# Kernel optimization log

Measured on AMD Instinct MI355X. Metric: run time of the kernel, lower is better.

The kernel has to match this reference:

```python
import jax, jax.numpy as jnp
import numpy as np
from jax import lax

B, L, D = 8, 2048, 512
K = 16            # cysteines per sequence (fixed by construction)
CYS = 4           # AA2ID['C']
CW = 5            # disulfide_context_window
KW = 2 * CW + 1   # conv kernel size = 11
H = D // 2        # LSTM hidden per direction = 256
STR = 0.4         # cys_optimization_strength


def setup_inputs() -> dict:
    key = jax.random.key(0)
    ks = jax.random.split(key, 16)
    hidden_states = jax.random.normal(ks[0], (B, L, D), jnp.float32)
    # amino-acid ids with exactly K cysteines per sequence, spaced > KW apart
    aa = jax.random.randint(ks[1], (B, L), 0, 20)
    aa = jnp.where(aa == CYS, 5, aa)
    base = 64 + 128 * jnp.arange(K)
    jitter = jax.random.randint(ks[2], (B, K), -40, 41)
    pos = base[None, :] + jitter  # [B,K], strictly increasing, gaps > 11
    aa_ids = aa.at[jnp.arange(B)[:, None], pos].set(CYS)
    s = 0.05
    W_bil = jax.random.normal(ks[3], (128, D, D)) * s
    b_bil = jax.random.normal(ks[4], (128,)) * s
    cls_w1 = jax.random.normal(ks[5], (64, 128)) * s
    cls_b1 = jax.random.normal(ks[6], (64,)) * s
    cls_w2 = jax.random.normal(ks[7], (1, 64)) * s
    cls_b2 = jax.random.normal(ks[8], (1,)) * s
    # 2 layers x 2 directions; both layers have input size D (2*H == D)
    lstm_Wih = jax.random.normal(ks[9], (2, 2, 4 * H, D)) * s
    lstm_Whh = jax.random.normal(ks[10], (2, 2, 4 * H, H)) * s
    lstm_bih = jax.random.normal(ks[11], (2, 2, 4 * H)) * s
    lstm_bhh = jax.random.normal(ks[12], (2, 2, 4 * H)) * s
    conv_w = jax.random.normal(ks[13], (D, D, KW)) * 0.02
    conv_b = jax.random.normal(ks[14], (D,)) * 0.02
    dsb_factor = jax.random.normal(ks[15], (D,)) * 0.1
    return dict(hidden_states=hidden_states, aa_ids=aa_ids, W_bil=W_bil,
                b_bil=b_bil, cls_w1=cls_w1, cls_b1=cls_b1, cls_w2=cls_w2,
                cls_b2=cls_b2, lstm_Wih=lstm_Wih, lstm_Whh=lstm_Whh,
                lstm_bih=lstm_bih, lstm_bhh=lstm_bhh, conv_w=conv_w,
                conv_b=conv_b, dsb_factor=dsb_factor)


def _lstm_dir(x, Wih, Whh, bih, bhh, reverse):
    # x: [B,L,In] -> [B,L,H]; PyTorch gate order i,f,g,o
    bsz = x.shape[0]
    xs = jnp.swapaxes(x, 0, 1)  # [L,B,In]
    if reverse:
        xs = xs[::-1]

    def step(carry, xt):
        h, c = carry
        g = xt @ Wih.T + h @ Whh.T + bih + bhh  # [B,4H]
        i, f, gg, o = jnp.split(g, 4, axis=-1)
        c = jax.nn.sigmoid(f) * c + jax.nn.sigmoid(i) * jnp.tanh(gg)
        h = jax.nn.sigmoid(o) * jnp.tanh(c)
        return (h, c), h

    init = (jnp.zeros((bsz, H), x.dtype), jnp.zeros((bsz, H), x.dtype))
    _, hs = lax.scan(step, init, xs)
    if reverse:
        hs = hs[::-1]
    return jnp.swapaxes(hs, 0, 1)


def _bilstm(x, Wih, Whh, bih, bhh):
    out = x
    for layer in range(2):  # dropout inactive in eval mode
        fw = _lstm_dir(out, Wih[layer, 0], Whh[layer, 0], bih[layer, 0], bhh[layer, 0], False)
        bw = _lstm_dir(out, Wih[layer, 1], Whh[layer, 1], bih[layer, 1], bhh[layer, 1], True)
        out = jnp.concatenate([fw, bw], axis=-1)
    return out


def reference(hidden_states, aa_ids, W_bil, b_bil, cls_w1, cls_b1, cls_w2,
              cls_b2, lstm_Wih, lstm_Whh, lstm_bih, lstm_bhh, conv_w, conv_b,
              dsb_factor):
    dt = hidden_states.dtype
    cys_mask = (aa_ids == CYS)  # [B,L] bool, exactly K per row
    pos = jax.vmap(lambda m: jnp.nonzero(m, size=K, fill_value=0)[0])(cys_mask)  # [B,K]

    # ---- batched bilinear + classifier over all cys pairs ----
    feats = jnp.take_along_axis(hidden_states, pos[:, :, None], axis=1)  # [B,K,D]
    t = jnp.einsum('bkd,cde->bkce', feats, W_bil)            # [B,K,128,D]
    pf = jnp.einsum('bkce,bme->bkmc', t, feats) + b_bil      # [B,K,K,128]
    h1 = jax.nn.relu(pf @ cls_w1.T + cls_b1)
    prob = jax.nn.sigmoid(h1 @ cls_w2.T + cls_b2)[..., 0]    # [B,K,K]
    dist = jnp.abs(pos[:, :, None] - pos[:, None, :])
    prob = jnp.where(dist < 2, prob * 0.1, prob)

    # ---- greedy NMS-style pair selection (prob desc, prob > 0.5, no reuse) ----
    iu, ju = jnp.triu_indices(K, k=1)  # P = K*(K-1)/2 pairs
    probs_flat = prob[:, iu, ju]       # [B,P]

    def greedy(pflat):
        order = jnp.argsort(-pflat)
        ii, jj, pp = iu[order], ju[order], pflat[order]

        def step(used, trip):
            i, j, p = trip
            sel = jnp.logical_and(jnp.logical_and(~used[i], ~used[j]), p > 0.5)
            used = used.at[i].set(used[i] | sel)
            used = used.at[j].set(used[j] | sel)
            return used, sel

        _, sels = lax.scan(step, jnp.zeros(K, bool), (ii, jj, pp))
        return jnp.zeros(iu.shape[0], bool).at[order].set(sels)

    sel_flat = jax.vmap(greedy)(probs_flat)
    sel_mat = jnp.zeros((B, K, K), bool).at[:, iu, ju].set(sel_flat)

    # ---- redox LSTM + windowed cys enhancement ----
    opt = _bilstm(hidden_states, lstm_Wih, lstm_Whh, lstm_bih, lstm_bhh)  # [B,L,D]
    cm = cys_mask.astype(dt)
    cov = lax.conv_general_dilated(cm[:, None, :], jnp.ones((1, 1, KW), dt),
                                   (1,), ((CW, CW),),
                                   dimension_numbers=('NCH', 'OIH', 'NCH'))[:, 0, :]
    win = (cov > 0).astype(dt)  # [B,L] 1 where within CW of a cysteine
    cys_enh = hidden_states + STR * opt * win[..., None] + dsb_factor * cm[..., None]

    # ---- local structure conv ----
    struct = lax.conv_general_dilated(jnp.swapaxes(cys_enh, 1, 2), conv_w,
                                      (1,), ((CW, CW),),
                                      dimension_numbers=('NCH', 'OIH', 'NCH'))
    struct = jnp.swapaxes(struct + conv_b[None, :, None], 1, 2)

    output = hidden_states + 0.3 * (cys_enh - hidden_states) + 0.2 * (struct - hidden_states)
    return (output, prob, sel_mat)
```

## Files before the change

kernel.cpp:

```cpp
#include <hip/hip_runtime.h>
#include <hip/hip_bf16.h>

typedef float  f32x4 __attribute__((ext_vector_type(4)));
typedef float  f32x2 __attribute__((ext_vector_type(2)));
typedef int    i32x4 __attribute__((ext_vector_type(4)));
typedef int    i32x8 __attribute__((ext_vector_type(8)));

#define NB   8
#define LSEQ 2048
#define DDIM 512
#define KC   16

__device__ __forceinline__ float rcp_(float x){ return __builtin_amdgcn_rcpf(x); }
__device__ __forceinline__ float ex2_(float x){ return __builtin_amdgcn_exp2f(x); }
__device__ __forceinline__ float clamp60(float x){ return fminf(fmaxf(x, -60.f), 60.f); }
__device__ __forceinline__ unsigned pk2(float a, float b){
    __hip_bfloat16 x=__float2bfloat16(a), y=__float2bfloat16(b);
    return (unsigned)*(unsigned short*)&x | ((unsigned)*(unsigned short*)&y<<16);
}

#define GLDS(gp, lp) __builtin_amdgcn_global_load_lds(                      \
    (__attribute__((address_space(1))) const void*)(gp),                   \
    (__attribute__((address_space(3))) void*)(lp), 16, 0, 0)

__global__ __launch_bounds__(256) void k_prep(const float* __restrict__ hidden, __hip_bfloat16* __restrict__ hbf,
                                              const float* __restrict__ Wih, __hip_bfloat16* __restrict__ wihbf,
                                              const float* __restrict__ bih, const float* __restrict__ bhh,
                                              float* __restrict__ bias2,
                                              const float* __restrict__ convw, __hip_bfloat16* __restrict__ wtc,
                                              const int* __restrict__ aa, int* __restrict__ pos,
                                              float* __restrict__ cm, float* __restrict__ win,
                                              int* __restrict__ cnt){
    int bid = blockIdx.x, tid = threadIdx.x;
    if(bid < 4096){
        size_t i = (size_t)bid*256 + tid;
        const f32x4* s = (const f32x4*)(hidden + i*8);
        f32x4 v0 = s[0], v1 = s[1];
        i32x4 o; o.x = pk2(v0.x,v0.y); o.y = pk2(v0.z,v0.w);
                 o.z = pk2(v1.x,v1.y); o.w = pk2(v1.z,v1.w);
        ((i32x4*)hbf)[i] = o;
    } else if(bid < 5120){
        size_t i = (size_t)(bid-4096)*256 + tid;
        const f32x4* s = (const f32x4*)(Wih + i*8);
        f32x4 v0 = s[0], v1 = s[1];
        i32x4 o; o.x = pk2(v0.x,v0.y); o.y = pk2(v0.z,v0.w);
                 o.z = pk2(v1.x,v1.y); o.w = pk2(v1.z,v1.w);
        ((i32x4*)wihbf)[i] = o;
    } else if(bid < 5136){
        int i = (bid-5120)*256 + tid;
        bias2[i] = bih[i] + bhh[i];
    } else if(bid < 6160){
        int idx = (bid-5136)*256 + tid;
        #pragma unroll
        for(int tap=0; tap<11; ++tap)
            wtc[(size_t)tap*262144 + idx] = __float2bfloat16(convw[(size_t)idx*11 + tap]);
    } else if(bid < 6168){
        int b = bid - 6160;
        __shared__ unsigned char fl[LSEQ];
        for(int t=tid; t<LSEQ; t+=256) fl[t] = (aa[b*LSEQ+t]==4) ? 1 : 0;
        __syncthreads();
        if(tid==0){
            int c=0;
            for(int t=0; t<LSEQ && c<KC; ++t) if(fl[t]) pos[b*KC + c++] = t;
            for(; c<KC; ++c) pos[b*KC+c]=0;
        }
        for(int t=tid; t<LSEQ; t+=256){
            cm[b*LSEQ+t] = fl[t] ? 1.f : 0.f;
            int lo = t-5 < 0 ? 0 : t-5;
            int hi = t+5 > LSEQ-1 ? LSEQ-1 : t+5;
            float wv = 0.f;
            for(int u=lo; u<=hi; ++u) if(fl[u]) wv = 1.f;
            win[b*LSEQ+t] = wv;
        }
    } else {
        if(tid < 256) cnt[tid] = 0;
    }
}

__device__ __forceinline__ void gemm_body(char* smem, const __hip_bfloat16* __restrict__ A,
        const __hip_bfloat16* __restrict__ Bw, const float* __restrict__ bias,
        __hip_bfloat16* __restrict__ C, int* __restrict__ cnt, int g){
    const int KD = 512, N = 2048;
    int nt = g & 15;
    int j  = g >> 4;
    int kpos = j >> 3, bat = j & 7;
    int mt = bat*16 + ((kpos&1) ? (15 - (kpos>>1)) : (kpos>>1));
    __hip_bfloat16 (*As)[32] = (__hip_bfloat16(*)[32])smem;
    __hip_bfloat16 (*Bs)[32] = (__hip_bfloat16(*)[32])(smem + 8192);
    int tid = threadIdx.x, w = tid>>6, lane = tid&63, lo = lane&15, hi = lane>>4;
    int wm = w>>1, wn = w&1;
    f32x4 acc[2][4];
    #pragma unroll
    for(int s=0;s<2;s++){
        #pragma unroll
        for(int t2=0;t2<4;t2++) acc[s][t2] = (f32x4){0.f,0.f,0.f,0.f};
    }
    int lr = tid>>2, lc = (tid&3)*8;
    const __hip_bfloat16* Ab = A  + (size_t)(mt*128)*KD;
    const __hip_bfloat16* Bb = Bw + (size_t)(nt*128)*KD;
    for(int kk=0; kk<KD; kk+=32){
        __builtin_amdgcn_s_barrier();
        GLDS(Ab + (size_t)lr*KD + kk + lc, &As[lr][lc]);
        GLDS(Bb + (size_t)lr*KD + kk + lc, &Bs[lr][lc]);
        asm volatile("s_waitcnt vmcnt(0)" ::: "memory");
        __builtin_amdgcn_s_barrier();
        i32x4 av[2], bv[4];
        #pragma unroll
        for(int s=0;s<2;s++) av[s] = *(const i32x4*)(&As[wm*32+s*16+lo][hi*8]);
        #pragma unroll
        for(int t2=0;t2<4;t2++) bv[t2] = *(const i32x4*)(&Bs[wn*64+t2*16+lo][hi*8]);
        asm volatile("s_nop 1" ::);
        #pragma unroll
        for(int s=0;s<2;s++){
            #pragma unroll
            for(int t2=0;t2<4;t2++)
                asm volatile("v_mfma_f32_16x16x32_bf16 %0, %1, %2, %0" : "+v"(acc[s][t2]) : "v"(av[s]), "v"(bv[t2]));
        }
    }
    asm volatile("s_nop 7\n\ts_nop 7" ::);
    #pragma unroll
    for(int t2=0;t2<4;t2++){
        int n = nt*128 + wn*64 + t2*16 + lo;
        float bn = bias[n];
        #pragma unroll
        for(int s=0;s<2;s++){
            #pragma unroll
            for(int rr=0;rr<4;rr++){
                int m = mt*128 + wm*32 + s*16 + hi*4 + rr;
                C[(size_t)m*N + n] = __float2bfloat16(acc[s][t2][rr] + bn);
            }
        }
    }
    asm volatile("s_waitcnt vmcnt(0)" ::: "memory");
    __syncthreads();
    if(tid==0)
        __hip_atomic_fetch_add(cnt + mt, 1, __ATOMIC_RELEASE, __HIP_MEMORY_SCOPE_AGENT);
}

__device__ __forceinline__ void recur_body(char* smem, const float* __restrict__ Whh,
        const __hip_bfloat16* __restrict__ Gx, __hip_bfloat16* __restrict__ Hout,
        const int* __restrict__ cnt, int layer, int bat, int dir){
    unsigned char (*hb)[256]    = (unsigned char(*)[256])smem;
    __hip_bfloat16 (*gxs)[1024] = (__hip_bfloat16(*)[1024])(smem + 512);
    const int tid = threadIdx.x, w = tid>>6, lane = tid&63, lo = lane&15, hi = lane>>4;
    for(int i=tid; i<128; i+=512) ((int*)smem)[i] = 0;

    i32x8 bf[8][2];
    const float* wbase = Whh + ((size_t)(layer*2 + dir)*1024)*256;
    #pragma unroll
    for(int q=0;q<4;q++){
        #pragma unroll
        for(int s=0;s<2;s++){
            int j = q*256 + w*32 + s*16 + lo;
            const float* wr = wbase + (size_t)j*256;
            #pragma unroll
            for(int c=0;c<2;c++){
                i32x8 v;
                #pragma unroll
                for(int u=0; u<8; ++u){
                    f32x4 wv = *(const f32x4*)(wr + c*128 + hi*32 + u*4);
                    int pk = __builtin_amdgcn_cvt_pk_fp8_f32(wv.x, wv.y, 0, false);
                    pk = __builtin_amdgcn_cvt_pk_fp8_f32(wv.z, wv.w, pk, true);
                    v[u] = pk;
                }
                bf[q*2+s][c] = v;
            }
        }
    }
    const int pm = w*32 + ((hi&1)<<4) + lo;
    float cst = 0.f;
    const __hip_bfloat16* gxbase = Gx + (size_t)bat*LSEQ*2048 + dir*1024;
    const int cbase = bat*16;
    int mtr = -1;

    {
        int tok0 = dir ? (LSEQ-1) : 0;
        int tok1 = dir ? (LSEQ-2) : 1;
        if(w < 2){
            int mtn = cbase + (tok0>>7);
            if(lane==0){
                while(__hip_atomic_load(cnt+mtn, __ATOMIC_ACQUIRE, __HIP_MEMORY_SCOPE_AGENT) < 16)
                    __builtin_amdgcn_s_sleep(2);
            }
            mtr = mtn;
            GLDS(gxbase + (size_t)tok0*2048 + w*512 + lane*8, &gxs[0][w*512]);
            GLDS(gxbase + (size_t)tok1*2048 + w*512 + lane*8, &gxs[1][w*512]);
        }
    }
    asm volatile("s_waitcnt vmcnt(0) lgkmcnt(0)" ::: "memory");
    __builtin_amdgcn_s_barrier();
    __builtin_amdgcn_sched_barrier(0);

    int cur = 0;
    for(int t=0; t<LSEQ; ++t){
        const int tt = dir ? (LSEQ-1-t) : t;
        const int hcur = t&1, hnxt = hcur^1;
        int nx2 = cur+2; if(nx2>=3) nx2-=3;
        float xi = __bfloat162float(gxs[cur][      pm]);
        float xf = __bfloat162float(gxs[cur][256 + pm]);
        float xg = __bfloat162float(gxs[cur][512 + pm]);
        float xo = __bfloat162float(gxs[cur][768 + pm]);
        {
            int tp = (t+2 < LSEQ) ? (t+2) : (LSEQ-1);
            int tok = dir ? (LSEQ-1-tp) : tp;
            if(w < 2){
                int mtn = cbase + (tok>>7);
                if(mtn != mtr){
                    if(lane==0){
                        while(__hip_atomic_load(cnt+mtn, __ATOMIC_ACQUIRE, __HIP_MEMORY_SCOPE_AGENT) < 16)
                            __builtin_amdgcn_s_sleep(2);
                    }
                    mtr = mtn;
                }
                GLDS(gxbase + (size_t)tok*2048 + w*512 + lane*8, &gxs[nx2][w*512]);
            }
        }
        i32x8 af[2];
        #pragma unroll
        for(int c=0;c<2;c++){
            i32x4 v0 = *(const i32x4*)(&hb[hcur][c*128 + hi*32]);
            i32x4 v1 = *(const i32x4*)(&hb[hcur][c*128 + hi*32 + 16]);
            af[c] = __builtin_shufflevector(v0, v1, 0,1,2,3,4,5,6,7);
        }
        f32x4 aa[8], ab[8];
        #pragma unroll
        for(int i=0;i<8;i++){ aa[i] = (f32x4){0.f,0.f,0.f,0.f}; ab[i] = (f32x4){0.f,0.f,0.f,0.f}; }
        asm volatile("s_nop 1" ::);
        #pragma unroll
        for(int i=0;i<8;i++)
            asm volatile("v_mfma_f32_16x16x128_f8f6f4 %0, %1, %2, %0"
                         : "+v"(aa[i]) : "v"(af[0]), "a"(bf[i][0]));
        #pragma unroll
        for(int i=0;i<8;i++)
            asm volatile("v_mfma_f32_16x16x128_f8f6f4 %0, %1, %2, %0"
                         : "+v"(ab[i]) : "v"(af[1]), "a"(bf[i][1]));
        asm volatile("s_nop 7\n\ts_nop 7" ::);
        {
            float aI = (hi&1) ? (aa[1][0]+ab[1][0]) : (aa[0][0]+ab[0][0]);
            float aF = (hi&1) ? (aa[3][0]+ab[3][0]) : (aa[2][0]+ab[2][0]);
            float aG = (hi&1) ? (aa[5][0]+ab[5][0]) : (aa[4][0]+ab[4][0]);
            float aO = (hi&1) ? (aa[7][0]+ab[7][0]) : (aa[6][0]+ab[6][0]);
            float gi = aI + xi;
            float gf = aF + xf;
            float gg = aG + xg;
            float go = aO + xo;
            float sf = rcp_(1.f + ex2_(gf * -1.44269504f));
            float ag = ex2_(clamp60(gg * 2.88539008f));
            float bi = ex2_(clamp60(gi * -1.44269504f));
            float it = (ag - 1.f) * rcp_((1.f + bi) * (ag + 1.f));
            float c  = sf*cst + it;
            cst = c;
            float ac = ex2_(clamp60(c * 2.88539008f));
            float bo = ex2_(clamp60(go * -1.44269504f));
            float h  = (ac - 1.f) * rcp_((1.f + bo) * (ac + 1.f));
            if(hi < 2){
                int pk = __builtin_amdgcn_cvt_pk_fp8_f32(h, h, 0, false);
                hb[hnxt][pm] = (unsigned char)(pk & 0xff);
                Hout[((size_t)bat*LSEQ + tt)*512 + dir*256 + pm] = __float2bfloat16(h);
            }
        }
        asm volatile("s_waitcnt vmcnt(2) lgkmcnt(0)" ::: "memory");
        __builtin_amdgcn_s_barrier();
        __builtin_amdgcn_sched_barrier(0);
        cur = (cur+1 == 3) ? 0 : cur+1;
    }
}

__device__ __forceinline__ void bilinear_body(char* smem, const float* __restrict__ hidden,
        const int* __restrict__ pos, const float* __restrict__ Wb, const float* __restrict__ bb,
        float* __restrict__ pf, int idx){
    int c = idx & 127, b = idx >> 7;
    float (*fl)[516] = (float(*)[516])smem;
    float (*tl)[516] = (float(*)[516])(smem + 33024);
    int tid = threadIdx.x;
    for(int i=tid; i<2048; i+=512){
        int k = i>>7, d = (i&127)*4;
        int p = pos[b*KC + k];
        f32x4 v = *(const f32x4*)(hidden + ((size_t)b*LSEQ + p)*DDIM + d);
        fl[k][d]=v.x; fl[k][d+1]=v.y; fl[k][d+2]=v.z; fl[k][d+3]=v.w;
    }
    __syncthreads();
    int e = tid;
    float acc[16];
    #pragma unroll
    for(int k=0;k<16;k++) acc[k]=0.f;
    const float* wc = Wb + (size_t)c*512*512;
    for(int d=0; d<512; ++d){
        float wv = wc[(size_t)d*512 + e];
        #pragma unroll
        for(int k=0;k<16;k++) acc[k] += fl[k][d]*wv;
    }
    #pragma unroll
    for(int k=0;k<16;k++) tl[k][e] = acc[k];
    __syncthreads();
    if(tid < 256){
        int kq = tid>>4, mq = tid&15;
        const f32x4* tp = (const f32x4*)&tl[kq][0];
        const f32x4* fp = (const f32x4*)&fl[mq][0];
        float s = 0.f;
        #pragma unroll 8
        for(int e2=0;e2<128;e2++){ f32x4 a=tp[e2], v=fp[e2]; s += a.x*v.x + a.y*v.y + a.z*v.z + a.w*v.w; }
        pf[(((size_t)b*16+kq)*16+mq)*128 + c] = s + bb[c];
    }
}

__device__ __forceinline__ void clsgreedy_body(char* smem, const float* __restrict__ pf,
        const float* __restrict__ w1, const float* __restrict__ b1,
        const float* __restrict__ w2, const float* __restrict__ b2,
        const int* __restrict__ pos, float* __restrict__ prob, float* __restrict__ sel, int b){
    float (*sw1)[128] = (float(*)[128])smem;
    float* sw2 = (float*)(smem + 32768);
    float* sb1 = sw2 + 64;
    float* sp  = sb1 + 64;
    unsigned char* si = (unsigned char*)(sp + 120);
    unsigned char* sj = si + 120;
    int tid = threadIdx.x;
    for(int i=tid; i<8192; i+=512) sw1[i>>7][i&127] = w1[i];
    if(tid<64){ sw2[tid]=w2[tid]; sb1[tid]=b1[tid]; }
    if(tid==0){
        int idx=0;
        for(int i=0;i<16;i++) for(int j=i+1;j<16;j++){ si[idx]=(unsigned char)i; sj[idx]=(unsigned char)j; idx++; }
    }
    if(tid<256) sel[b*256+tid] = 0.f;
    __syncthreads();
    if(tid < 256){
        int k = tid>>4, m = tid&15;
        const f32x4* pp = (const f32x4*)(pf + (((size_t)b*16+k)*16+m)*128);
        f32x4 pr[32];
        #pragma unroll
        for(int i=0;i<32;i++) pr[i] = pp[i];
        float lg = b2[0];
        for(int n=0;n<64;n++){
            const f32x4* wr = (const f32x4*)&sw1[n][0];
            float a = sb1[n];
            #pragma unroll
            for(int i=0;i<32;i++){ f32x4 wv = wr[i]; a += pr[i].x*wv.x + pr[i].y*wv.y + pr[i].z*wv.z + pr[i].w*wv.w; }
            a = fmaxf(a, 0.f);
            lg += a*sw2[n];
        }
        float p = rcp_(1.f + ex2_(lg * -1.44269504f));
        int dk = pos[b*16+k]-pos[b*16+m]; if(dk<0) dk=-dk;
        if(dk<2) p *= 0.1f;
        prob[b*256 + k*16 + m] = p;
        if(k < m) sp[k*(31-k)/2 + (m-k-1)] = p;
    }
    __syncthreads();
    if(tid==0){
        bool done[120]; bool used[16];
        for(int i=0;i<120;i++) done[i]=false;
        for(int i=0;i<16;i++)  used[i]=false;
        for(int it=0; it<120; ++it){
            int bi=-1; float bp=-1e30f;
            for(int q=0;q<120;q++) if(!done[q] && sp[q]>bp){ bp=sp[q]; bi=q; }
            done[bi]=true;
            if(bp>0.5f && !used[si[bi]] && !used[sj[bi]]){
                used[si[bi]]=true; used[sj[bi]]=true;
                sel[b*256 + si[bi]*16 + sj[bi]] = 1.f;
            }
        }
    }
}

__global__ __launch_bounds__(512) void k_fused1(const float* __restrict__ Whh, __hip_bfloat16* __restrict__ Gx,
        __hip_bfloat16* __restrict__ Hout, int* __restrict__ cnt,
        const __hip_bfloat16* __restrict__ hbf, const __hip_bfloat16* __restrict__ wihbf,
        const float* __restrict__ bias2,
        const float* __restrict__ hidden, const int* __restrict__ pos,
        const float* __restrict__ Wbil, const float* __restrict__ bbil, float* __restrict__ pf){
    __shared__ __attribute__((aligned(16))) char smem[98304];
    int bid = blockIdx.x;
    if(bid < 16){
        recur_body(smem, Whh, Gx, Hout, cnt, 0, bid>>1, bid&1);
    } else if(bid < 16 + 2048){
        gemm_body(smem, hbf, wihbf, bias2, Gx, cnt, bid - 16);
    } else {
        bilinear_body(smem, hidden, pos, Wbil, bbil, pf, bid - 2064);
    }
}

__global__ __launch_bounds__(512) void k_fused2(const float* __restrict__ Whh, __hip_bfloat16* __restrict__ Gx,
        __hip_bfloat16* __restrict__ Hout, int* __restrict__ cnt,
        const __hip_bfloat16* __restrict__ out1, const __hip_bfloat16* __restrict__ wihbf,
        const float* __restrict__ bias2,
        const float* __restrict__ pf, const float* __restrict__ w1, const float* __restrict__ b1,
        const float* __restrict__ w2, const float* __restrict__ b2, const int* __restrict__ pos,
        float* __restrict__ prob, float* __restrict__ sel){
    __shared__ __attribute__((aligned(16))) char smem[98304];
    int bid = blockIdx.x;
    if(bid < 16){
        recur_body(smem, Whh, Gx, Hout, cnt, 1, bid>>1, bid&1);
    } else if(bid < 16 + 2048){
        gemm_body(smem, out1, wihbf + (size_t)2048*512, bias2 + 2048, Gx, cnt, bid - 16);
    } else {
        clsgreedy_body(smem, pf, w1, b1, w2, b2, pos, prob, sel, bid - 2064);
    }
}

__global__ __launch_bounds__(256) void k_convce(const float* __restrict__ hs, const __hip_bfloat16* __restrict__ opt,
        const float* __restrict__ win, const float* __restrict__ cm, const float* __restrict__ dsb,
        const __hip_bfloat16* __restrict__ wt, const float* __restrict__ convb, float* __restrict__ outp){
    int mt = blockIdx.x & 31, b = blockIdx.x >> 5;
    __shared__ __hip_bfloat16 S[74][520];
    int tid = threadIdx.x;
    for(int i=tid; i<74*64; i+=256){
        int rq = i>>6, cc = (i&63)*8;
        int tok = mt*64 - 5 + rq;
        i32x4 o = (i32x4){0,0,0,0};
        if(tok>=0 && tok<LSEQ){
            size_t base = ((size_t)b*LSEQ + tok)*512 + cc;
            float wv = win[b*LSEQ+tok]*0.4f, cv = cm[b*LSEQ+tok];
            f32x4 h0 = *(const f32x4*)(hs + base);
            f32x4 h1 = *(const f32x4*)(hs + base + 4);
            unsigned long long u0 = *(const unsigned long long*)(opt + base);
            unsigned long long u1 = *(const unsigned long long*)(opt + base + 4);
            f32x4 d0 = *(const f32x4*)(dsb + cc);
            f32x4 d1 = *(const f32x4*)(dsb + cc + 4);
            float c0 = h0.x + wv*__uint_as_float((unsigned)(u0      & 0xffffull)<<16) + d0.x*cv;
            float c1 = h0.y + wv*__uint_as_float((unsigned)((u0>>16)& 0xffffull)<<16) + d0.y*cv;
            float c2 = h0.z + wv*__uint_as_float((unsigned)((u0>>32)& 0xffffull)<<16) + d0.z*cv;
            float c3 = h0.w + wv*__uint_as_float((unsigned)((u0>>48)& 0xffffull)<<16) + d0.w*cv;
            float c4 = h1.x + wv*__uint_as_float((unsigned)(u1      & 0xffffull)<<16) + d1.x*cv;
            float c5 = h1.y + wv*__uint_as_float((unsigned)((u1>>16)& 0xffffull)<<16) + d1.y*cv;
            float c6 = h1.z + wv*__uint_as_float((unsigned)((u1>>32)& 0xffffull)<<16) + d1.z*cv;
            float c7 = h1.w + wv*__uint_as_float((unsigned)((u1>>48)& 0xffffull)<<16) + d1.w*cv;
            o.x = pk2(c0,c1); o.y = pk2(c2,c3); o.z = pk2(c4,c5); o.w = pk2(c6,c7);
        }
        *(i32x4*)(&S[rq][cc]) = o;
    }
    __syncthreads();
    int w = tid>>6, lane = tid&63, lo = lane&15, hi = lane>>4;
    f32x4 acc[4][8];
    #pragma unroll
    for(int ms=0;ms<4;ms++){
        #pragma unroll
        for(int s=0;s<8;s++) acc[ms][s] = (f32x4){0.f,0.f,0.f,0.f};
    }
    asm volatile("s_nop 1" ::);
    for(int tap=0; tap<11; ++tap){
        const __hip_bfloat16* wtp = wt + (size_t)tap*262144 + (size_t)(w*128)*512;
        for(int kk=0; kk<512; kk+=32){
            i32x4 a[4];
            #pragma unroll
            for(int ms=0;ms<4;ms++) a[ms] = *(const i32x4*)(&S[ms*16 + lo + tap][kk + hi*8]);
            #pragma unroll
            for(int s=0;s<8;s++){
                i32x4 bq = *(const i32x4*)(wtp + (size_t)(s*16 + lo)*512 + kk + hi*8);
                #pragma unroll
                for(int ms=0;ms<4;ms++)
                    asm volatile("v_mfma_f32_16x16x32_bf16 %0, %1, %2, %0" : "+v"(acc[ms][s]) : "v"(a[ms]), "v"(bq));
            }
        }
    }
    asm volatile("s_nop 7\n\ts_nop 7" ::);
    #pragma unroll
    for(int s=0;s<8;s++){
        int co = w*128 + s*16 + lo;
        float cb = convb[co];
        #pragma unroll
        for(int ms=0;ms<4;ms++){
            #pragma unroll
            for(int rr=0; rr<4; ++rr){
                int row = ms*16 + hi*4 + rr;
                int tok = mt*64 + row;
                size_t gi = ((size_t)b*LSEQ + tok)*512 + co;
                float h   = hs[gi];
                float cef = __bfloat162float(S[row + 5][co]);
                outp[gi] = 0.5f*h + 0.3f*cef + 0.2f*(acc[ms][s][rr] + cb);
            }
        }
    }
}

extern "C" void kernel_launch(void* const* d_in, const int* in_sizes, int n_in,
                              void* d_out, int out_size, void* d_ws, size_t ws_size,
                              hipStream_t stream)
{
    (void)in_sizes; (void)n_in; (void)out_size; (void)ws_size;
    const float* hidden = (const float*)d_in[0];
    const int*   aa     = (const int*)d_in[1];
    const float* Wbil   = (const float*)d_in[2];
    const float* bbil   = (const float*)d_in[3];
    const float* w1     = (const float*)d_in[4];
    const float* b1     = (const float*)d_in[5];
    const float* w2     = (const float*)d_in[6];
    const float* b2     = (const float*)d_in[7];
    const float* Wih    = (const float*)d_in[8];
    const float* Whh    = (const float*)d_in[9];
    const float* bih    = (const float*)d_in[10];
    const float* bhh    = (const float*)d_in[11];
    const float* convw  = (const float*)d_in[12];
    const float* convb  = (const float*)d_in[13];
    const float* dsb    = (const float*)d_in[14];

    float* outp = (float*)d_out;
    float* prob = outp + (size_t)NB*LSEQ*DDIM;
    float* sel  = prob + NB*KC*KC;

    char* p = (char*)d_ws;
    auto alloc = [&](size_t bytes)->char*{ char* r = p; p += (bytes + 255) & ~(size_t)255; return r; };
    __hip_bfloat16* gx    = (__hip_bfloat16*)alloc((size_t)16384*2048*2);
    __hip_bfloat16* hbf   = (__hip_bfloat16*)alloc((size_t)NB*LSEQ*DDIM*2);
    __hip_bfloat16* wihbf = (__hip_bfloat16*)alloc((size_t)2*2048*512*2);
    float*          bias2 = (float*)        alloc((size_t)2*2048*4);
    __hip_bfloat16* out1  = (__hip_bfloat16*)alloc((size_t)NB*LSEQ*DDIM*2);
    __hip_bfloat16* out2  = (__hip_bfloat16*)alloc((size_t)NB*LSEQ*DDIM*2);
    __hip_bfloat16* wtc   = (__hip_bfloat16*)alloc((size_t)11*512*512*2);
    float*          pf    = (float*)        alloc((size_t)NB*KC*KC*128*4);
    int*            pos   = (int*)          alloc((size_t)NB*KC*4);
    float*          cm    = (float*)        alloc((size_t)NB*LSEQ*4);
    float*          win   = (float*)        alloc((size_t)NB*LSEQ*4);
    int*            cnt1  = (int*)          alloc((size_t)256*4);
    int*            cnt2  = cnt1 + 128;

    k_prep<<<6169, 256, 0, stream>>>(hidden, hbf, Wih, wihbf, bih, bhh, bias2, convw, wtc, aa, pos, cm, win, cnt1);
    k_fused1<<<16 + 2048 + 1024, 512, 0, stream>>>(Whh, gx, out1, cnt1, hbf, wihbf, bias2,
                                                   hidden, pos, Wbil, bbil, pf);
    k_fused2<<<16 + 2048 + 8, 512, 0, stream>>>(Whh, gx, out2, cnt2, out1, wihbf, bias2,
                                                pf, w1, b1, w2, b2, pos, prob, sel);
    k_convce<<<256, 256, 0, stream>>>(hidden, out2, win, cm, dsb, wtc, convb, outp);
}
```

Measured before the change: 4.067 ms.

## Interleave LSTM gate rows so each lane loads its four gate preactivations directly

```diff
diff --git a/kernel.cpp b/kernel.cpp
--- a/kernel.cpp
+++ b/kernel.cpp
@@ -14,6 +14,8 @@
 __device__ __forceinline__ float rcp_(float x){ return __builtin_amdgcn_rcpf(x); }
 __device__ __forceinline__ float ex2_(float x){ return __builtin_amdgcn_exp2f(x); }
 __device__ __forceinline__ float clamp60(float x){ return fminf(fmaxf(x, -60.f), 60.f); }
+__device__ __forceinline__ float blo(unsigned u){ return __uint_as_float(u<<16); }
+__device__ __forceinline__ float bhi(unsigned u){ return __uint_as_float(u & 0xffff0000u); }
 __device__ __forceinline__ unsigned pk2(float a, float b){
     __hip_bfloat16 x=__float2bfloat16(a), y=__float2bfloat16(b);
     return (unsigned)*(unsigned short*)&x | ((unsigned)*(unsigned short*)&y<<16);
@@ -40,15 +42,25 @@
                  o.z = pk2(v1.x,v1.y); o.w = pk2(v1.z,v1.w);
         ((i32x4*)hbf)[i] = o;
     } else if(bid < 5120){
-        size_t i = (size_t)(bid-4096)*256 + tid;
-        const f32x4* s = (const f32x4*)(Wih + i*8);
+        size_t o = ((size_t)(bid-4096)*256 + tid) * 8;
+        int Rp  = (int)(o >> 9);
+        int col = (int)(o & 511);
+        int lp  = Rp >> 10;
+        int base= Rp & 1023;
+        int p = base >> 2, q = base & 3;
+        int Rs = (lp<<10) + (q<<8) + p;
+        const f32x4* s = (const f32x4*)(Wih + ((size_t)Rs << 9) + col);
         f32x4 v0 = s[0], v1 = s[1];
-        i32x4 o; o.x = pk2(v0.x,v0.y); o.y = pk2(v0.z,v0.w);
-                 o.z = pk2(v1.x,v1.y); o.w = pk2(v1.z,v1.w);
-        ((i32x4*)wihbf)[i] = o;
+        i32x4 oo; oo.x = pk2(v0.x,v0.y); oo.y = pk2(v0.z,v0.w);
+                  oo.z = pk2(v1.x,v1.y); oo.w = pk2(v1.z,v1.w);
+        ((i32x4*)wihbf)[o>>3] = oo;
     } else if(bid < 5136){
         int i = (bid-5120)*256 + tid;
-        bias2[i] = bih[i] + bhh[i];
+        int l = i >> 11, b2 = i & 2047;
+        int dir = b2 >> 10, b = b2 & 1023;
+        int p = b >> 2, q = b & 3;
+        int src = ((l*2+dir)<<10) + (q<<8) + p;
+        bias2[i] = bih[src] + bhh[src];
     } else if(bid < 6160){
         int idx = (bid-5136)*256 + tid;
         #pragma unroll
@@ -140,8 +152,7 @@
 __device__ __forceinline__ void recur_body(char* smem, const float* __restrict__ Whh,
         const __hip_bfloat16* __restrict__ Gx, __hip_bfloat16* __restrict__ Hout,
         const int* __restrict__ cnt, int layer, int bat, int dir){
-    unsigned char (*hb)[256]    = (unsigned char(*)[256])smem;
-    __hip_bfloat16 (*gxs)[1024] = (__hip_bfloat16(*)[1024])(smem + 512);
+    unsigned char (*hb)[256] = (unsigned char(*)[256])smem;
     const int tid = threadIdx.x, w = tid>>6, lane = tid&63, lo = lane&15, hi = lane>>4;
     for(int i=tid; i<128; i+=512) ((int*)smem)[i] = 0;
 
@@ -169,51 +180,43 @@
     }
     const int pm = w*32 + ((hi&1)<<4) + lo;
     float cst = 0.f;
-    const __hip_bfloat16* gxbase = Gx + (size_t)bat*LSEQ*2048 + dir*1024;
+    const __hip_bfloat16* gxb = Gx + (size_t)bat*LSEQ*2048 + dir*1024;
     const int cbase = bat*16;
     int mtr = -1;
 
+    uint2 gc, gn;
     {
         int tok0 = dir ? (LSEQ-1) : 0;
         int tok1 = dir ? (LSEQ-2) : 1;
-        if(w < 2){
-            int mtn = cbase + (tok0>>7);
-            if(lane==0){
-                while(__hip_atomic_load(cnt+mtn, __ATOMIC_ACQUIRE, __HIP_MEMORY_SCOPE_AGENT) < 16)
-                    __builtin_amdgcn_s_sleep(2);
-            }
-            mtr = mtn;
-            GLDS(gxbase + (size_t)tok0*2048 + w*512 + lane*8, &gxs[0][w*512]);
-            GLDS(gxbase + (size_t)tok1*2048 + w*512 + lane*8, &gxs[1][w*512]);
-        }
-    }
-    asm volatile("s_waitcnt vmcnt(0) lgkmcnt(0)" ::: "memory");
+        int mtn = cbase + (tok0>>7);
+        if(lane==0){
+            while(__hip_atomic_load(cnt+mtn, __ATOMIC_ACQUIRE, __HIP_MEMORY_SCOPE_AGENT) < 16)
+                __builtin_amdgcn_s_sleep(2);
+        }
+        mtr = mtn;
+        gc = *(const uint2*)(gxb + (size_t)tok0*2048 + pm*4);
+        gn = *(const uint2*)(gxb + (size_t)tok1*2048 + pm*4);
+    }
+    asm volatile("s_waitcnt lgkmcnt(0)" ::: "memory");
     __builtin_amdgcn_s_barrier();
     __builtin_amdgcn_sched_barrier(0);
 
-    int cur = 0;
     for(int t=0; t<LSEQ; ++t){
         const int tt = dir ? (LSEQ-1-t) : t;
         const int hcur = t&1, hnxt = hcur^1;
-        int nx2 = cur+2; if(nx2>=3) nx2-=3;
-        float xi = __bfloat162float(gxs[cur][      pm]);
-        float xf = __bfloat162float(gxs[cur][256 + pm]);
-        float xg = __bfloat162float(gxs[cur][512 + pm]);
-        float xo = __bfloat162float(gxs[cur][768 + pm]);
+        uint2 gf2;
         {
             int tp = (t+2 < LSEQ) ? (t+2) : (LSEQ-1);
             int tok = dir ? (LSEQ-1-tp) : tp;
-            if(w < 2){
-                int mtn = cbase + (tok>>7);
-                if(mtn != mtr){
-                    if(lane==0){
-                        while(__hip_atomic_load(cnt+mtn, __ATOMIC_ACQUIRE, __HIP_MEMORY_SCOPE_AGENT) < 16)
-                            __builtin_amdgcn_s_sleep(2);
-                    }
-                    mtr = mtn;
+            int mtn = cbase + (tok>>7);
+            if(mtn != mtr){
+                if(lane==0){
+                    while(__hip_atomic_load(cnt+mtn, __ATOMIC_ACQUIRE, __HIP_MEMORY_SCOPE_AGENT) < 16)
+                        __builtin_amdgcn_s_sleep(2);
                 }
-                GLDS(gxbase + (size_t)tok*2048 + w*512 + lane*8, &gxs[nx2][w*512]);
-            }
+                mtr = mtn;
+            }
+            gf2 = *(const uint2*)(gxb + (size_t)tok*2048 + pm*4);
         }
         i32x8 af[2];
         #pragma unroll
@@ -240,10 +243,10 @@
             float aF = (hi&1) ? (aa[3][0]+ab[3][0]) : (aa[2][0]+ab[2][0]);
             float aG = (hi&1) ? (aa[5][0]+ab[5][0]) : (aa[4][0]+ab[4][0]);
             float aO = (hi&1) ? (aa[7][0]+ab[7][0]) : (aa[6][0]+ab[6][0]);
-            float gi = aI + xi;
-            float gf = aF + xf;
-            float gg = aG + xg;
-            float go = aO + xo;
+            float gi = aI + blo(gc.x);
+            float gf = aF + bhi(gc.x);
+            float gg = aG + blo(gc.y);
+            float go = aO + bhi(gc.y);
             float sf = rcp_(1.f + ex2_(gf * -1.44269504f));
             float ag = ex2_(clamp60(gg * 2.88539008f));
             float bi = ex2_(clamp60(gi * -1.44269504f));
@@ -259,10 +262,10 @@
                 Hout[((size_t)bat*LSEQ + tt)*512 + dir*256 + pm] = __float2bfloat16(h);
             }
         }
-        asm volatile("s_waitcnt vmcnt(2) lgkmcnt(0)" ::: "memory");
+        asm volatile("s_waitcnt lgkmcnt(0)" ::: "memory");
         __builtin_amdgcn_s_barrier();
         __builtin_amdgcn_sched_barrier(0);
-        cur = (cur+1 == 3) ? 0 : cur+1;
+        gc = gn; gn = gf2;
     }
 }
 
```

Measured after the change: 4.054 ms. No clear change (-0.3%).
